# Kernel optimization log

Measured on AMD Instinct MI355X. Metric: run time of the kernel, lower is better.

## Reference

```python
import jax, jax.numpy as jnp
import numpy as np

N = 50          # n_nodes
TAU = 1.0       # sinkhorn_tau
ITERS = 5       # sinkhorn_iters
ALPHA = 1.0


def _psi_fn(x, W1, b1, W2, b2):
    # x: [B, N, F]
    h = jax.nn.leaky_relu(x @ W1 + b1)          # [B, N, H], slope 0.01 matches torch default
    M = jax.nn.leaky_relu(h @ W2 + b2)          # [B, N, N]
    P = jnp.exp(M / TAU)
    for _ in range(ITERS):                      # alternating row/col normalization
        P = P / jnp.sum(P, axis=2, keepdims=True)
        P = P / jnp.sum(P, axis=1, keepdims=True)
    return P


def _hungarian(cost):
    """O(n^3) Hungarian (shortest augmenting path, like scipy.linear_sum_assignment).
    cost: [n, n] numpy. Returns col index assigned to each row (minimizes cost)."""
    n = cost.shape[0]
    INF = 1e18
    u = np.zeros(n + 1)
    v = np.zeros(n + 1)
    p = np.zeros(n + 1, dtype=np.int64)   # p[j] = row matched to column j (1-based)
    for i in range(1, n + 1):
        p[0] = i
        j0 = 0
        minv = np.full(n + 1, INF)
        way = np.zeros(n + 1, dtype=np.int64)
        used = np.zeros(n + 1, dtype=bool)
        while True:
            used[j0] = True
            i0 = p[j0]
            cur = cost[i0 - 1, :] - u[i0] - v[1:]
            free = ~used[1:]
            better = free & (cur < minv[1:])
            mv = minv[1:]
            mv[better] = cur[better]
            way[1:][better] = j0
            cand = np.where(free, mv, INF)
            j1 = int(np.argmin(cand)) + 1
            delta = cand[j1 - 1]
            u[p[used]] += delta
            v[used] -= delta
            mv[free] -= delta
            j0 = j1
            if p[j0] == 0:
                break
        while j0 != 0:
            j1 = way[j0]
            p[j0] = p[j1]
            j0 = j1
    row_to_col = np.zeros(n, dtype=np.int64)
    for j in range(1, n + 1):
        if p[j] > 0:
            row_to_col[p[j] - 1] = j - 1
    return row_to_col


def setup_inputs() -> dict:
    key = jax.random.key(0)
    k1, k2, k3, k4, k5 = jax.random.split(key, 5)
    B, F, H = 128, 1024, 4096
    s1 = 1.0 / np.sqrt(F)
    s2 = 1.0 / np.sqrt(H)
    x = jax.random.normal(k1, (B, N, F), dtype=jnp.float32)
    W1 = jax.random.uniform(k2, (F, H), minval=-s1, maxval=s1, dtype=jnp.float32)
    b1 = jax.random.uniform(k3, (H,), minval=-s1, maxval=s1, dtype=jnp.float32)
    W2 = jax.random.uniform(k4, (H, N), minval=-s2, maxval=s2, dtype=jnp.float32)
    b2 = jax.random.uniform(k5, (N,), minval=-s2, maxval=s2, dtype=jnp.float32)
    return {"x": x, "W1": W1, "b1": b1, "W2": W2, "b2": b2, "do_round": 1}


def reference(x, W1, b1, W2, b2, do_round):
    psi = _psi_fn(x, W1, b1, W2, b2)            # [B, N, N] doubly-stochastic (approx)
    if do_round:
        batch = np.asarray(psi)
        B = batch.shape[0]
        perms_np = np.zeros((B, N, N), dtype=np.float32)
        rows = np.arange(N)
        for i in range(B):
            cols = _hungarian(-batch[i])        # maximize psi == minimize -psi
            perms_np[i, rows, cols] = 1.0
        perms = jnp.asarray(perms_np)
        dist = jnp.sum(psi * perms, axis=(1, 2)) / N   # [B]
        X = (1.0 - ALPHA) * perms + ALPHA * psi
        return (psi, perms, X, dist)
    return (psi, None, None, None)
```

## Files before the change

### kernel.cpp

```cpp
#include <hip/hip_runtime.h>

#define NMAT 50
#define BATCH 128
#define FDIM 1024
#define HDIM 4096
#define ROWS 6400
#define PSIZE 320000
#define NPART 16
#define HINF 1e18

#define WS_M_OFF   0
#define WS_XH_OFF  20480000LL
#define WS_XL_OFF  33587200LL
#define WS_W1H_OFF 46694400LL
#define WS_W1L_OFF 55083008LL
#define WS_W2H_OFF 63471616LL
#define WS_W2L_OFF 63995904LL
#define WS_H_OFF   64520192LL
#define WS_MIN     (WS_H_OFF + 128LL * HDIM * 4)

typedef __bf16 bf16x8 __attribute__((ext_vector_type(8)));
typedef short short8 __attribute__((ext_vector_type(8)));
typedef float f32x4 __attribute__((ext_vector_type(4)));
typedef unsigned short u16;
typedef unsigned int u32;

__device__ __forceinline__ float bf16_to_f32(unsigned short h) {
  return __uint_as_float(((unsigned int)h) << 16);
}
__device__ __forceinline__ unsigned short f32_to_bf16(float f) {
  unsigned int u = __float_as_uint(f);
  u += 0x7FFFu + ((u >> 16) & 1u);
  return (unsigned short)(u >> 16);
}

__device__ __forceinline__ void gload16(const u16* g, u16* l) {
  __builtin_amdgcn_global_load_lds(
      (const __attribute__((address_space(1))) unsigned int*)g,
      (__attribute__((address_space(3))) unsigned int*)l, 16, 0, 0);
}

__device__ __forceinline__ double wave_min_f64(double x) {
  union { double d; int i[2]; } u, t;
  u.d = x;
#define DPP_MIN_STEP(ctrl)                                                   \
  t.i[0] = __builtin_amdgcn_update_dpp(u.i[0], u.i[0], ctrl, 0xf, 0xf, false);\
  t.i[1] = __builtin_amdgcn_update_dpp(u.i[1], u.i[1], ctrl, 0xf, 0xf, false);\
  u.d = fmin(u.d, t.d);
  DPP_MIN_STEP(0x111)
  DPP_MIN_STEP(0x112)
  DPP_MIN_STEP(0x114)
  DPP_MIN_STEP(0x118)
  DPP_MIN_STEP(0x142)
  DPP_MIN_STEP(0x143)
#undef DPP_MIN_STEP
  union { double d; int i[2]; } r;
  r.i[0] = __builtin_amdgcn_readlane(u.i[0], 63);
  r.i[1] = __builtin_amdgcn_readlane(u.i[1], 63);
  return r.d;
}

__device__ __forceinline__ double readlane_f64(double x, int l) {
  union { double d; int i2[2]; } a, b;
  a.d = x;
  b.i2[0] = __builtin_amdgcn_readlane(a.i2[0], l);
  b.i2[1] = __builtin_amdgcn_readlane(a.i2[1], l);
  return b.d;
}

__global__ __launch_bounds__(256) void convert_x(
    const float* __restrict__ X, u16* __restrict__ Xh, u16* __restrict__ Xl) {
  int t = threadIdx.x;
  int mt = blockIdx.x >> 5, k0b = blockIdx.x & 31;
  size_t outbase = (size_t)blockIdx.x * 4096;
#pragma unroll
  for (int it = 0; it < 2; ++it) {
    int idx = t + it * 256;
    int m = idx & 127, kg = idx >> 7;
    const float* src = X + (size_t)(mt * 128 + m) * FDIM + k0b * 32 + kg * 8;
    float4 v0 = *(const float4*)src;
    float4 v1 = *(const float4*)(src + 4);
    float f[8] = {v0.x, v0.y, v0.z, v0.w, v1.x, v1.y, v1.z, v1.w};
    unsigned short h[8], l[8];
#pragma unroll
    for (int j = 0; j < 8; ++j) {
      h[j] = f32_to_bf16(f[j]);
      l[j] = f32_to_bf16(f[j] - bf16_to_f32(h[j]));
    }
    uint4 hv, lv;
    hv.x = h[0] | ((unsigned)h[1] << 16); hv.y = h[2] | ((unsigned)h[3] << 16);
    hv.z = h[4] | ((unsigned)h[5] << 16); hv.w = h[6] | ((unsigned)h[7] << 16);
    lv.x = l[0] | ((unsigned)l[1] << 16); lv.y = l[2] | ((unsigned)l[3] << 16);
    lv.z = l[4] | ((unsigned)l[5] << 16); lv.w = l[6] | ((unsigned)l[7] << 16);
    size_t off = outbase + (size_t)(kg * 128 + m) * 8;
    *(uint4*)&Xh[off] = hv;
    *(uint4*)&Xl[off] = lv;
  }
}

__global__ __launch_bounds__(256) void convert_w1(
    const float* __restrict__ W1, u16* __restrict__ Wh, u16* __restrict__ Wl) {
  int t = threadIdx.x;
  int nt = blockIdx.x >> 5, k0b = blockIdx.x & 31;
  size_t outbase = (size_t)blockIdx.x * 4096;
#pragma unroll
  for (int it = 0; it < 2; ++it) {
    int idx = t + it * 256;
    int n = idx & 127, kg = idx >> 7;
    float f[8];
#pragma unroll
    for (int j = 0; j < 8; ++j)
      f[j] = W1[(size_t)(k0b * 32 + kg * 8 + j) * HDIM + nt * 128 + n];
    unsigned short h[8], l[8];
#pragma unroll
    for (int j = 0; j < 8; ++j) {
      h[j] = f32_to_bf16(f[j]);
      l[j] = f32_to_bf16(f[j] - bf16_to_f32(h[j]));
    }
    uint4 hv, lv;
    hv.x = h[0] | ((unsigned)h[1] << 16); hv.y = h[2] | ((unsigned)h[3] << 16);
    hv.z = h[4] | ((unsigned)h[5] << 16); hv.w = h[6] | ((unsigned)h[7] << 16);
    lv.x = l[0] | ((unsigned)l[1] << 16); lv.y = l[2] | ((unsigned)l[3] << 16);
    lv.z = l[4] | ((unsigned)l[5] << 16); lv.w = l[6] | ((unsigned)l[7] << 16);
    size_t off = outbase + (size_t)(kg * 128 + n) * 8;
    *(uint4*)&Wh[off] = hv;
    *(uint4*)&Wl[off] = lv;
  }
}

__global__ __launch_bounds__(256) void convert_w2(
    const float* __restrict__ W2, u16* __restrict__ W2h, u16* __restrict__ W2l) {
  int idx = blockIdx.x * 256 + threadIdx.x;
  int n = idx >> 12, k = idx & 4095;
  float f = (n < NMAT) ? W2[(size_t)k * NMAT + n] : 0.0f;
  unsigned short hi = f32_to_bf16(f);
  unsigned short lo = f32_to_bf16(f - bf16_to_f32(hi));
  W2h[idx] = hi;
  W2l[idx] = lo;
}

__global__ __launch_bounds__(256) void gemm1_mfma(
    const u16* __restrict__ Ah_, const u16* __restrict__ Al_,
    const u16* __restrict__ Bh_, const u16* __restrict__ Bl_,
    const float* __restrict__ b1,
    u32* __restrict__ HTout,
    int mt0, int stride) {
  __shared__ __align__(16) u16 Ah[4096];
  __shared__ __align__(16) u16 Al[4096];
  __shared__ __align__(16) u16 Bh[4096];
  __shared__ __align__(16) u16 Bl[4096];
  int t = threadIdx.x;
  int wave = t >> 6, lane = t & 63;
  int nt = blockIdx.x & 31;
  int mtl = blockIdx.x >> 5;
  int wm = wave >> 1, wn = wave & 1;
  int fr = lane & 15, fg = lane >> 4;

  f32x4 acc[4][4];
#pragma unroll
  for (int i = 0; i < 4; ++i)
#pragma unroll
    for (int j = 0; j < 4; ++j) acc[i][j] = (f32x4){0.f, 0.f, 0.f, 0.f};

  const u16* pAh = Ah_ + (size_t)(mt0 + mtl) * 32 * 4096;
  const u16* pAl = Al_ + (size_t)(mt0 + mtl) * 32 * 4096;
  const u16* pBh = Bh_ + (size_t)nt * 32 * 4096;
  const u16* pBl = Bl_ + (size_t)nt * 32 * 4096;
  int so = wave * 1024 + lane * 8;
  int ld = wave * 1024;

  for (int k0b = 0; k0b < 32; ++k0b) {
    __syncthreads();
    size_t sb = (size_t)k0b * 4096;
    gload16(pAh + sb + so,       &Ah[ld]);
    gload16(pAh + sb + so + 512, &Ah[ld + 512]);
    gload16(pAl + sb + so,       &Al[ld]);
    gload16(pAl + sb + so + 512, &Al[ld + 512]);
    gload16(pBh + sb + so,       &Bh[ld]);
    gload16(pBh + sb + so + 512, &Bh[ld + 512]);
    gload16(pBl + sb + so,       &Bl[ld]);
    gload16(pBl + sb + so + 512, &Bl[ld + 512]);
    __syncthreads();
    bf16x8 ah[4], al[4], bh[4], bl[4];
#pragma unroll
    for (int i = 0; i < 4; ++i) {
      int arow = (fg * 128 + wm * 64 + i * 16 + fr) * 8;
      ah[i] = *(const bf16x8*)&Ah[arow];
      al[i] = *(const bf16x8*)&Al[arow];
      int brow = (fg * 128 + wn * 64 + i * 16 + fr) * 8;
      bh[i] = *(const bf16x8*)&Bh[brow];
      bl[i] = *(const bf16x8*)&Bl[brow];
    }
#pragma unroll
    for (int i = 0; i < 4; ++i)
#pragma unroll
      for (int j = 0; j < 4; ++j)
        acc[i][j] = __builtin_amdgcn_mfma_f32_16x16x32_bf16(ah[i], bh[j], acc[i][j], 0, 0, 0);
#pragma unroll
    for (int i = 0; i < 4; ++i)
#pragma unroll
      for (int j = 0; j < 4; ++j)
        acc[i][j] = __builtin_amdgcn_mfma_f32_16x16x32_bf16(ah[i], bl[j], acc[i][j], 0, 0, 0);
#pragma unroll
    for (int i = 0; i < 4; ++i)
#pragma unroll
      for (int j = 0; j < 4; ++j)
        acc[i][j] = __builtin_amdgcn_mfma_f32_16x16x32_bf16(al[i], bh[j], acc[i][j], 0, 0, 0);
  }

  int colb = nt * 128 + wn * 64 + fr;
  int rowb = mtl * 128 + wm * 64 + fg * 4;
#pragma unroll
  for (int j = 0; j < 4; ++j) {
    float bias = b1[colb + j * 16];
#pragma unroll
    for (int i = 0; i < 4; ++i) {
      uint4 pk;
      u32* pp = &pk.x;
#pragma unroll
      for (int r = 0; r < 4; ++r) {
        float v = acc[i][j][r] + bias;
        v = v >= 0.0f ? v : 0.01f * v;
        unsigned short hi = f32_to_bf16(v);
        unsigned short lo = f32_to_bf16(v - bf16_to_f32(hi));
        pp[r] = ((u32)hi << 16) | lo;
      }
      *(uint4*)&HTout[(size_t)(colb + j * 16) * stride + rowb + i * 16] = pk;
    }
  }
}

__global__ __launch_bounds__(64) void gemm2_bf16(
    const u32* __restrict__ hT,
    const u16* __restrict__ W2h,
    const u16* __restrict__ W2l,
    float* __restrict__ Mpart,
    int row0, int stride) {
  int lane = threadIdx.x;
  int kz = blockIdx.y;
  int fr = lane & 15, fg = lane >> 4;

  f32x4 acc[4];
#pragma unroll
  for (int nt = 0; nt < 4; ++nt) acc[nt] = (f32x4){0.f, 0.f, 0.f, 0.f};

  const u32* hA = hT + blockIdx.x * 16 + fr;
  const int kbase = kz * 256;
  u32 hp[8], hn[8];
#pragma unroll
  for (int kk = 0; kk < 8; ++kk)
    hp[kk] = hA[(size_t)(kbase + fg * 8 + kk) * stride];
#pragma unroll
  for (int kk = 0; kk < 8; ++kk)
    hn[kk] = hA[(size_t)(kbase + 32 + fg * 8 + kk) * stride];

  for (int ks = 0; ks < 8; ++ks) {
    int k0 = kbase + ks * 32;
    u32 h2[8];
    if (ks < 6) {
#pragma unroll
      for (int kk = 0; kk < 8; ++kk)
        h2[kk] = hA[(size_t)(k0 + 64 + fg * 8 + kk) * stride];
    }
    short8 hs, ls;
#pragma unroll
    for (int kk = 0; kk < 8; ++kk) {
      hs[kk] = (short)(hp[kk] >> 16);
      ls[kk] = (short)(hp[kk] & 0xffffu);
    }
    bf16x8 ah = *(bf16x8*)&hs;
    bf16x8 al = *(bf16x8*)&ls;
#pragma unroll
    for (int nt = 0; nt < 4; ++nt) {
      const size_t boff = (size_t)(nt * 16 + fr) * 4096 + k0 + fg * 8;
      bf16x8 bh = *(const bf16x8*)&W2h[boff];
      bf16x8 bl = *(const bf16x8*)&W2l[boff];
      acc[nt] = __builtin_amdgcn_mfma_f32_16x16x32_bf16(ah, bh, acc[nt], 0, 0, 0);
      acc[nt] = __builtin_amdgcn_mfma_f32_16x16x32_bf16(ah, bl, acc[nt], 0, 0, 0);
      acc[nt] = __builtin_amdgcn_mfma_f32_16x16x32_bf16(al, bh, acc[nt], 0, 0, 0);
    }
    if (ks < 7) {
#pragma unroll
      for (int kk = 0; kk < 8; ++kk) hp[kk] = hn[kk];
    }
    if (ks < 6) {
#pragma unroll
      for (int kk = 0; kk < 8; ++kk) hn[kk] = h2[kk];
    }
  }

  float* Mout = Mpart + (size_t)kz * PSIZE;
  int rowbase = row0 + blockIdx.x * 16 + fg * 4;
#pragma unroll
  for (int nt = 0; nt < 4; ++nt) {
    int col = nt * 16 + fr;
    if (col < NMAT) {
#pragma unroll
      for (int r = 0; r < 4; ++r)
        Mout[(size_t)(rowbase + r) * NMAT + col] = acc[nt][r];
    }
  }
}

__global__ __launch_bounds__(64) void sinkhorn_hungarian(
    const float* __restrict__ Mpart, const float* __restrict__ b2,
    float* __restrict__ out_psi, float* __restrict__ out_X,
    float* __restrict__ out_perms, float* __restrict__ out_dist) {
  int b = blockIdx.x, lane = threadIdx.x;
  __shared__ double P[2500];
  __shared__ double cost[2500];
  __shared__ double rs[50];
  __shared__ double u[51];
  __shared__ int p[51];
  __shared__ int wayl[51];
  const size_t base = (size_t)b * 2500;

  for (int e = lane; e < 2500; e += 64) {
    double m = 0.0;
#pragma unroll
    for (int pz = 0; pz < NPART; ++pz)
      m += (double)Mpart[(size_t)pz * PSIZE + base + e];
    m += (double)b2[e % 50];
    m = m >= 0.0 ? m : 0.01 * m;
    P[e] = exp(m);
  }
  __syncthreads();
  for (int it = 0; it < 5; ++it) {
    if (lane < 50) { double s = 0; for (int j = 0; j < 50; ++j) s += P[lane * 50 + j]; rs[lane] = s; }
    __syncthreads();
    for (int e = lane; e < 2500; e += 64) P[e] /= rs[e / 50];
    __syncthreads();
    if (lane < 50) { double s = 0; for (int r = 0; r < 50; ++r) s += P[r * 50 + lane]; rs[lane] = s; }
    __syncthreads();
    for (int e = lane; e < 2500; e += 64) P[e] /= rs[e % 50];
    __syncthreads();
  }
  for (int e = lane; e < 2500; e += 64) {
    float f = (float)P[e];
    out_psi[base + e] = f;
    out_X[base + e] = f;
    cost[e] = -P[e];
  }
  if (lane < 51) { u[lane] = 0.0; p[lane] = 0; }
  __syncthreads();

  double v = 0.0;
  bool lactive = lane < NMAT;
  for (int i = 1; i <= NMAT; ++i) {
    int pc = (lane <= 50) ? p[lane] : 0;
    double uc = (lane < 50) ? u[lane + 1] : 0.0;
    bool used = false;
    int way = 0;
    int j0 = 0, j1 = 0;
    double uacc = 0.0, total = 0.0;
    for (int guard = 0; guard < 64; ++guard) {
      if (lane == j0 - 1) used = true;
      int j0u = __builtin_amdgcn_readfirstlane(j0);
      int i0 = (j0u == 0) ? i : __builtin_amdgcn_readlane(pc, j0u);
      double ui0 = readlane_f64(uc, i0 - 1);
      double cand = HINF;
      if (lactive && !used) {
        cand = cost[(i0 - 1) * NMAT + lane] - ui0 - v;
        way = j0;
      }
      double m = wave_min_f64(cand);
      unsigned long long bal = __ballot(cand == m);
      j1 = (int)__builtin_ctzll(bal) + 1;
      if (used) { v -= m; uacc += m; }
      total += m;
      j0 = j1;
      int j1u = __builtin_amdgcn_readfirstlane(j0);
      if (__builtin_amdgcn_readlane(pc, j1u) == 0) break;
    }
    if (used && lactive) u[p[lane + 1]] += uacc;
    if (lane == 63) u[i] += total;
    if (lactive) wayl[lane + 1] = way;
    __syncthreads();
    if (lane == 0) {
      int j = j1;
      for (int step = 0; step < 64 && j != 0; ++step) {
        int jw = wayl[j];
        p[j] = (jw == 0) ? i : p[jw];
        j = jw;
      }
    }
    __syncthreads();
  }

  size_t pbase = (size_t)b * 2500;
  for (int e = lane; e < 2500; e += 64) out_perms[pbase + e] = 0.0f;
  __syncthreads();
  double val = 0.0;
  if (lactive) {
    int row = p[lane + 1] - 1;
    if (row < 0) row = 0;
    if (row > 49) row = 49;
    out_perms[pbase + (size_t)row * NMAT + lane] = 1.0f;
    val = P[(size_t)row * NMAT + lane];
  }
#pragma unroll
  for (int s = 32; s > 0; s >>= 1) val += __shfl_xor(val, s, 64);
  if (lane == 0) out_dist[b] = (float)(val / (double)NMAT);
}

extern "C" void kernel_launch(void* const* d_in, const int* in_sizes, int n_in,
                              void* d_out, int out_size, void* d_ws, size_t ws_size,
                              hipStream_t stream) {
  const float* x  = (const float*)d_in[0];
  const float* W1 = (const float*)d_in[1];
  const float* b1 = (const float*)d_in[2];
  const float* W2 = (const float*)d_in[3];
  const float* b2 = (const float*)d_in[4];
  float* out = (float*)d_out;
  float* out_psi   = out;
  float* out_perms = out + PSIZE;
  float* out_X     = out + 2 * PSIZE;
  float* out_dist  = out + 3 * PSIZE;

  if (ws_size < (size_t)WS_MIN) return;

  char* ws = (char*)d_ws;
  float* Mpart = (float*)(ws + WS_M_OFF);
  u16* Xh  = (u16*)(ws + WS_XH_OFF);
  u16* Xl  = (u16*)(ws + WS_XL_OFF);
  u16* W1h = (u16*)(ws + WS_W1H_OFF);
  u16* W1l = (u16*)(ws + WS_W1L_OFF);
  u16* W2h = (u16*)(ws + WS_W2H_OFF);
  u16* W2l = (u16*)(ws + WS_W2L_OFF);
  u32* hbuf = (u32*)(ws + WS_H_OFF);
  long long avail = (long long)ws_size - WS_H_OFF;
  int max_rows = (int)(avail / (HDIM * 4));
  max_rows = (max_rows / 128) * 128;
  if (max_rows > ROWS) max_rows = ROWS;

  hipLaunchKernelGGL(convert_x, dim3(1600), dim3(256), 0, stream, x, Xh, Xl);
  hipLaunchKernelGGL(convert_w1, dim3(1024), dim3(256), 0, stream, W1, W1h, W1l);
  hipLaunchKernelGGL(convert_w2, dim3(1024), dim3(256), 0, stream, W2, W2h, W2l);

  for (int r0 = 0; r0 < ROWS; r0 += max_rows) {
    int rows = (ROWS - r0 < max_rows) ? (ROWS - r0) : max_rows;
    hipLaunchKernelGGL(gemm1_mfma, dim3((rows / 128) * 32), dim3(256), 0, stream,
                       Xh, Xl, W1h, W1l, b1, hbuf, r0 / 128, rows);
    hipLaunchKernelGGL(gemm2_bf16, dim3(rows / 16, NPART), dim3(64), 0, stream,
                       hbuf, W2h, W2l, Mpart, r0, rows);
  }
  hipLaunchKernelGGL(sinkhorn_hungarian, dim3(BATCH), dim3(64), 0, stream,
                     Mpart, b2, out_psi, out_X, out_perms, out_dist);
}
```

Baseline: 460.8 us.

## Store hidden activations row-major and use f32 fast-path min in Hungarian

The hidden activation buffer now has a row-major [rows, HDIM] layout instead of a transposed one. gemm2 can then read each lane's 8 consecutive k values with two 16-byte vector loads instead of 8 strided scalar loads. The cost moves to gemm1's epilogue, which now writes scalar u32 values with column-strided addresses instead of packed uint4 stores. Separately, the Hungarian argmin first runs a cheaper f32 DPP wave reduction and falls back to the f64 reduction only when several lanes tie in f32. The fast path adds a ballot and popcount on every step.

```diff
diff --git a/kernel.cpp b/kernel.cpp
--- a/kernel.cpp
+++ b/kernel.cpp
@@ -60,6 +60,22 @@
   return r.d;
 }
 
+__device__ __forceinline__ float wave_min_f32(float x) {
+  float t;
+#define DPP_MINF_STEP(ctrl)                                                  \
+  t = __uint_as_float(__builtin_amdgcn_update_dpp(                           \
+      (int)__float_as_uint(x), (int)__float_as_uint(x), ctrl, 0xf, 0xf, false));\
+  x = fminf(x, t);
+  DPP_MINF_STEP(0x111)
+  DPP_MINF_STEP(0x112)
+  DPP_MINF_STEP(0x114)
+  DPP_MINF_STEP(0x118)
+  DPP_MINF_STEP(0x142)
+  DPP_MINF_STEP(0x143)
+#undef DPP_MINF_STEP
+  return __uint_as_float(__builtin_amdgcn_readlane((int)__float_as_uint(x), 63));
+}
+
 __device__ __forceinline__ double readlane_f64(double x, int l) {
   union { double d; int i2[2]; } a, b;
   a.d = x;
@@ -143,8 +159,8 @@
     const u16* __restrict__ Ah_, const u16* __restrict__ Al_,
     const u16* __restrict__ Bh_, const u16* __restrict__ Bl_,
     const float* __restrict__ b1,
-    u32* __restrict__ HTout,
-    int mt0, int stride) {
+    u32* __restrict__ HRout,
+    int mt0) {
   __shared__ __align__(16) u16 Ah[4096];
   __shared__ __align__(16) u16 Al[4096];
   __shared__ __align__(16) u16 Bh[4096];
@@ -215,27 +231,25 @@
     float bias = b1[colb + j * 16];
 #pragma unroll
     for (int i = 0; i < 4; ++i) {
-      uint4 pk;
-      u32* pp = &pk.x;
 #pragma unroll
       for (int r = 0; r < 4; ++r) {
         float v = acc[i][j][r] + bias;
         v = v >= 0.0f ? v : 0.01f * v;
         unsigned short hi = f32_to_bf16(v);
         unsigned short lo = f32_to_bf16(v - bf16_to_f32(hi));
-        pp[r] = ((u32)hi << 16) | lo;
+        HRout[(size_t)(rowb + i * 16 + r) * HDIM + colb + j * 16] =
+            ((u32)hi << 16) | lo;
       }
-      *(uint4*)&HTout[(size_t)(colb + j * 16) * stride + rowb + i * 16] = pk;
     }
   }
 }
 
 __global__ __launch_bounds__(64) void gemm2_bf16(
-    const u32* __restrict__ hT,
+    const u32* __restrict__ hR,
     const u16* __restrict__ W2h,
     const u16* __restrict__ W2l,
     float* __restrict__ Mpart,
-    int row0, int stride) {
+    int row0) {
   int lane = threadIdx.x;
   int kz = blockIdx.y;
   int fr = lane & 15, fg = lane >> 4;
@@ -244,24 +258,21 @@
 #pragma unroll
   for (int nt = 0; nt < 4; ++nt) acc[nt] = (f32x4){0.f, 0.f, 0.f, 0.f};
 
-  const u32* hA = hT + blockIdx.x * 16 + fr;
+  const u32* hA = hR + (size_t)(blockIdx.x * 16 + fr) * HDIM + fg * 8;
   const int kbase = kz * 256;
-  u32 hp[8], hn[8];
-#pragma unroll
-  for (int kk = 0; kk < 8; ++kk)
-    hp[kk] = hA[(size_t)(kbase + fg * 8 + kk) * stride];
-#pragma unroll
-  for (int kk = 0; kk < 8; ++kk)
-    hn[kk] = hA[(size_t)(kbase + 32 + fg * 8 + kk) * stride];
+  uint4 c0 = *(const uint4*)&hA[kbase];
+  uint4 c1 = *(const uint4*)&hA[kbase + 4];
+  uint4 n0 = *(const uint4*)&hA[kbase + 32];
+  uint4 n1 = *(const uint4*)&hA[kbase + 36];
 
   for (int ks = 0; ks < 8; ++ks) {
     int k0 = kbase + ks * 32;
-    u32 h2[8];
+    uint4 f0 = {0, 0, 0, 0}, f1 = {0, 0, 0, 0};
     if (ks < 6) {
-#pragma unroll
-      for (int kk = 0; kk < 8; ++kk)
-        h2[kk] = hA[(size_t)(k0 + 64 + fg * 8 + kk) * stride];
-    }
+      f0 = *(const uint4*)&hA[k0 + 64];
+      f1 = *(const uint4*)&hA[k0 + 68];
+    }
+    u32 hp[8] = {c0.x, c0.y, c0.z, c0.w, c1.x, c1.y, c1.z, c1.w};
     short8 hs, ls;
 #pragma unroll
     for (int kk = 0; kk < 8; ++kk) {
@@ -279,14 +290,8 @@
       acc[nt] = __builtin_amdgcn_mfma_f32_16x16x32_bf16(ah, bl, acc[nt], 0, 0, 0);
       acc[nt] = __builtin_amdgcn_mfma_f32_16x16x32_bf16(al, bh, acc[nt], 0, 0, 0);
     }
-    if (ks < 7) {
-#pragma unroll
-      for (int kk = 0; kk < 8; ++kk) hp[kk] = hn[kk];
-    }
-    if (ks < 6) {
-#pragma unroll
-      for (int kk = 0; kk < 8; ++kk) hn[kk] = h2[kk];
-    }
+    if (ks < 7) { c0 = n0; c1 = n1; }
+    if (ks < 6) { n0 = f0; n1 = f1; }
   }
 
   float* Mout = Mpart + (size_t)kz * PSIZE;
@@ -363,9 +368,20 @@
         cand = cost[(i0 - 1) * NMAT + lane] - ui0 - v;
         way = j0;
       }
-      double m = wave_min_f64(cand);
-      unsigned long long bal = __ballot(cand == m);
-      j1 = (int)__builtin_ctzll(bal) + 1;
+      float cf = (float)cand;
+      float mf = wave_min_f32(cf);
+      unsigned long long balf = __ballot(cf == mf);
+      double m;
+      if (__builtin_popcountll(balf) == 1) {
+        int lmin = (int)__builtin_ctzll(balf);
+        m = readlane_f64(cand, lmin);
+        j1 = lmin + 1;
+      } else {
+        double candt = (cf == mf) ? cand : HINF;
+        m = wave_min_f64(candt);
+        unsigned long long bal = __ballot(cand == m);
+        j1 = (int)__builtin_ctzll(bal) + 1;
+      }
       if (used) { v -= m; uacc += m; }
       total += m;
       j0 = j1;
@@ -440,9 +456,9 @@
   for (int r0 = 0; r0 < ROWS; r0 += max_rows) {
     int rows = (ROWS - r0 < max_rows) ? (ROWS - r0) : max_rows;
     hipLaunchKernelGGL(gemm1_mfma, dim3((rows / 128) * 32), dim3(256), 0, stream,
-                       Xh, Xl, W1h, W1l, b1, hbuf, r0 / 128, rows);
+                       Xh, Xl, W1h, W1l, b1, hbuf, r0 / 128);
     hipLaunchKernelGGL(gemm2_bf16, dim3(rows / 16, NPART), dim3(64), 0, stream,
-                       hbuf, W2h, W2l, Mpart, r0, rows);
+                       hbuf, W2h, W2l, Mpart, r0);
   }
   hipLaunchKernelGGL(sinkhorn_hungarian, dim3(BATCH), dim3(64), 0, stream,
                      Mpart, b2, out_psi, out_X, out_perms, out_dist);
```

New measurement: 474.2 us. +2.9%, slower.

## Prefetch W2 fragments in GEMM2 and use f32 fast-path min in Hungarian

Applied to the files above, without the earlier changes.

The second GEMM now loads the next k-step's W2 high/low bf16 fragments into registers one iteration ahead, overlapping global loads with MFMA work. The Hungarian loop drops the separate shared cost array and reads -P directly. Its per-step wave argmin is first done in float with a cheaper DPP reduction, falling back to the double-precision reduction only when several lanes tie at the float minimum. This cuts latency on the serial critical path, at the cost of more registers and a possible extra reduction on ties.

```diff
diff --git a/kernel.cpp b/kernel.cpp
--- a/kernel.cpp
+++ b/kernel.cpp
@@ -60,6 +60,22 @@
   return r.d;
 }
 
+__device__ __forceinline__ float wave_min_f32(float x) {
+  float t;
+#define DPP_MINF_STEP(ctrl)                                                  \
+  t = __uint_as_float(__builtin_amdgcn_update_dpp(                           \
+      (int)__float_as_uint(x), (int)__float_as_uint(x), ctrl, 0xf, 0xf, false));\
+  x = fminf(x, t);
+  DPP_MINF_STEP(0x111)
+  DPP_MINF_STEP(0x112)
+  DPP_MINF_STEP(0x114)
+  DPP_MINF_STEP(0x118)
+  DPP_MINF_STEP(0x142)
+  DPP_MINF_STEP(0x143)
+#undef DPP_MINF_STEP
+  return __uint_as_float(__builtin_amdgcn_readlane((int)__float_as_uint(x), 63));
+}
+
 __device__ __forceinline__ double readlane_f64(double x, int l) {
   union { double d; int i2[2]; } a, b;
   a.d = x;
@@ -254,13 +270,32 @@
   for (int kk = 0; kk < 8; ++kk)
     hn[kk] = hA[(size_t)(kbase + 32 + fg * 8 + kk) * stride];
 
+  bf16x8 bhc[4], blc[4];
+#pragma unroll
+  for (int nt = 0; nt < 4; ++nt) {
+    const size_t boff = (size_t)(nt * 16 + fr) * 4096 + kbase + fg * 8;
+    bhc[nt] = *(const bf16x8*)&W2h[boff];
+    blc[nt] = *(const bf16x8*)&W2l[boff];
+  }
+
   for (int ks = 0; ks < 8; ++ks) {
     int k0 = kbase + ks * 32;
+    uint4 f0 = {0, 0, 0, 0}, f1 = {0, 0, 0, 0};
+    (void)f0; (void)f1;
     u32 h2[8];
     if (ks < 6) {
 #pragma unroll
       for (int kk = 0; kk < 8; ++kk)
         h2[kk] = hA[(size_t)(k0 + 64 + fg * 8 + kk) * stride];
+    }
+    bf16x8 bhn[4], bln[4];
+    if (ks < 7) {
+#pragma unroll
+      for (int nt = 0; nt < 4; ++nt) {
+        const size_t boff = (size_t)(nt * 16 + fr) * 4096 + k0 + 32 + fg * 8;
+        bhn[nt] = *(const bf16x8*)&W2h[boff];
+        bln[nt] = *(const bf16x8*)&W2l[boff];
+      }
     }
     short8 hs, ls;
 #pragma unroll
@@ -272,16 +307,15 @@
     bf16x8 al = *(bf16x8*)&ls;
 #pragma unroll
     for (int nt = 0; nt < 4; ++nt) {
-      const size_t boff = (size_t)(nt * 16 + fr) * 4096 + k0 + fg * 8;
-      bf16x8 bh = *(const bf16x8*)&W2h[boff];
-      bf16x8 bl = *(const bf16x8*)&W2l[boff];
-      acc[nt] = __builtin_amdgcn_mfma_f32_16x16x32_bf16(ah, bh, acc[nt], 0, 0, 0);
-      acc[nt] = __builtin_amdgcn_mfma_f32_16x16x32_bf16(ah, bl, acc[nt], 0, 0, 0);
-      acc[nt] = __builtin_amdgcn_mfma_f32_16x16x32_bf16(al, bh, acc[nt], 0, 0, 0);
+      acc[nt] = __builtin_amdgcn_mfma_f32_16x16x32_bf16(ah, bhc[nt], acc[nt], 0, 0, 0);
+      acc[nt] = __builtin_amdgcn_mfma_f32_16x16x32_bf16(ah, blc[nt], acc[nt], 0, 0, 0);
+      acc[nt] = __builtin_amdgcn_mfma_f32_16x16x32_bf16(al, bhc[nt], acc[nt], 0, 0, 0);
     }
     if (ks < 7) {
 #pragma unroll
       for (int kk = 0; kk < 8; ++kk) hp[kk] = hn[kk];
+#pragma unroll
+      for (int nt = 0; nt < 4; ++nt) { bhc[nt] = bhn[nt]; blc[nt] = bln[nt]; }
     }
     if (ks < 6) {
 #pragma unroll
@@ -308,7 +342,6 @@
     float* __restrict__ out_perms, float* __restrict__ out_dist) {
   int b = blockIdx.x, lane = threadIdx.x;
   __shared__ double P[2500];
-  __shared__ double cost[2500];
   __shared__ double rs[50];
   __shared__ double u[51];
   __shared__ int p[51];
@@ -339,7 +372,6 @@
     float f = (float)P[e];
     out_psi[base + e] = f;
     out_X[base + e] = f;
-    cost[e] = -P[e];
   }
   if (lane < 51) { u[lane] = 0.0; p[lane] = 0; }
   __syncthreads();
@@ -360,12 +392,23 @@
       double ui0 = readlane_f64(uc, i0 - 1);
       double cand = HINF;
       if (lactive && !used) {
-        cand = cost[(i0 - 1) * NMAT + lane] - ui0 - v;
+        cand = -P[(i0 - 1) * NMAT + lane] - ui0 - v;
         way = j0;
       }
-      double m = wave_min_f64(cand);
-      unsigned long long bal = __ballot(cand == m);
-      j1 = (int)__builtin_ctzll(bal) + 1;
+      float cf = (float)cand;
+      float mf = wave_min_f32(cf);
+      unsigned long long balf = __ballot(cf == mf);
+      double m;
+      if (__builtin_popcountll(balf) == 1) {
+        int lmin = (int)__builtin_ctzll(balf);
+        m = readlane_f64(cand, lmin);
+        j1 = lmin + 1;
+      } else {
+        double candt = (cf == mf) ? cand : HINF;
+        m = wave_min_f64(candt);
+        unsigned long long bal = __ballot(cand == m);
+        j1 = (int)__builtin_ctzll(bal) + 1;
+      }
       if (used) { v -= m; uacc += m; }
       total += m;
       j0 = j1;
```

After: 476.0 us. 3.3% more time.
